# Kernel optimization log

Hardware: AMD Instinct MI355X
Metric: run time of the kernel (lower is better)

The kernel has to match this reference:

```python
import jax, jax.numpy as jnp
import numpy as np

D = 300      # d_model / entity_embed_size, hard-coded in the module
TOPK = 20    # k in torch.topk


def setup_inputs() -> dict:
    key = jax.random.key(0)
    ks = jax.random.split(key, 6)
    N, T = 2, 4096
    scale = 1.0 / np.sqrt(D).astype(np.float32)
    return {
        "querys": jax.random.normal(ks[0], (N, T, D), jnp.float32),
        "keys":   jax.random.normal(ks[1], (N, T, D), jnp.float32),
        "values": jax.random.normal(ks[2], (N, T, D), jnp.float32),
        "Wq": jax.random.normal(ks[3], (D, D), jnp.float32) * scale,
        "Wk": jax.random.normal(ks[4], (D, D), jnp.float32) * scale,
        "Wv": jax.random.normal(ks[5], (D, D), jnp.float32) * scale,
        "num_heads": 6,
    }


def reference(querys, keys, values, Wq, Wk, Wv, num_heads):
    N, Tq, d = querys.shape
    h = int(num_heads)
    dh = d // h  # head dim (must divide; 300/6 = 50)

    # nn.Linear(bias=False): y = x @ W^T
    Q = querys @ Wq.T
    K = keys @ Wk.T
    V = values @ Wv.T  # computed but unused by the 'selected' attention, kept for fidelity

    # torch.cat(torch.split(X, dh, dim=2), dim=0): head index becomes major batch dim
    def to_heads(X):
        n, t, _ = X.shape
        return X.reshape(n, t, h, dh).transpose(2, 0, 1, 3).reshape(h * n, t, dh)

    Q_, K_ = to_heads(Q), to_heads(K)

    # scaled_dot_selected_product_attention
    scores = jnp.einsum('bqd,bkd->bqk', Q_, K_) / (dh ** 0.5)  # [hN, Tq, Tk]
    max_att = scores.max(axis=1)                                # [hN, Tk] (max over queries)
    top_vals, top_ids = jax.lax.top_k(max_att, TOPK)            # [hN, 20]
    probs = jax.nn.softmax(top_vals, axis=-1)                   # [hN, 20]
    # gather from K (not V!), matching the original code
    sel = jnp.take_along_axis(K_, top_ids[:, :, None], axis=1)  # [hN, 20, dh]
    out = jnp.sum(sel * probs[:, :, None], axis=1, keepdims=True)  # [hN, 1, dh]

    # torch.cat(torch.split(outputs, N, dim=0), dim=2): merge heads back on feature dim
    out = out.reshape(h, N, 1, dh).transpose(1, 2, 0, 3).reshape(N, 1, d)
    return out
```

## Files before the change

### kernel.cpp

```cpp
#include <hip/hip_runtime.h>
#include <hip/hip_bf16.h>
#include <math.h>

#define T      4096
#define Dm     300
#define NH     6
#define DH     50
#define NB     2
#define NBATCH 12
#define KTOP   20
#define NCAND  48
#define QC     8
#define RQC    16
#define KP     320
#define JP     304
#define NBINS  4096
#define BMAX   1024

typedef short  bs8  __attribute__((ext_vector_type(8)));
typedef float  f4   __attribute__((ext_vector_type(4)));

static __device__ __forceinline__ unsigned short f2bf(float f) {
    union { float f; unsigned u; } x{f};
    unsigned r = x.u + 0x7fffu + ((x.u >> 16) & 1u);
    return (unsigned short)(r >> 16);
}
static __device__ __forceinline__ float bf2f(unsigned short h) {
    union { unsigned u; float f; } x;
    x.u = ((unsigned)h) << 16;
    return x.f;
}
static __device__ __forceinline__ unsigned fkey(float f) {
    unsigned u = __float_as_uint(f);
    return (u & 0x80000000u) ? ~u : (u | 0x80000000u);
}

__global__ __launch_bounds__(256) void splitw_kernel(
    const float* __restrict__ Wq, const float* __restrict__ Wk,
    unsigned short* __restrict__ Wh, unsigned short* __restrict__ Wl)
{
    int idx = blockIdx.x * 256 + threadIdx.x;
    if (idx >= 2 * JP * KP) return;
    int z = idx / (JP * KP), rem = idx % (JP * KP);
    int row = rem / KP, k = rem % KP;
    const float* W = z ? Wk : Wq;
    float v = (row < 300 && k < 300) ? W[row * 300 + k] : 0.f;
    unsigned short h = f2bf(v);
    float r = v - bf2f(h);
    Wh[idx] = h;
    Wl[idx] = f2bf(r);
}

__global__ __launch_bounds__(256) void proj_mfma_kernel(
    const float* __restrict__ Xq, const float* __restrict__ Xk,
    const unsigned short* __restrict__ Wh, const unsigned short* __restrict__ Wl,
    float* __restrict__ Qt, float* __restrict__ Kt)
{
    __shared__ unsigned short Bh[16][KP + 8];
    __shared__ unsigned short Bl[16][KP + 8];

    const int z = blockIdx.z;
    const float* X  = z ? Xk : Xq;
    float*       Yt = z ? Kt : Qt;
    const unsigned short* WhB = Wh + (size_t)z * JP * KP;
    const unsigned short* WlB = Wl + (size_t)z * JP * KP;

    const int m0  = blockIdx.x * 128;
    const int j0  = blockIdx.y * 16;
    const int tid = threadIdx.x;
    const int wave = tid >> 6, lane = tid & 63;
    const int m16 = lane & 15, quad = lane >> 4;

    for (int i = tid; i < 16 * 40; i += 256) {
        int row = i / 40, c = i % 40;
        *(bs8*)&Bh[row][c * 8] = *(const bs8*)(WhB + (size_t)(j0 + row) * KP + c * 8);
        *(bs8*)&Bl[row][c * 8] = *(const bs8*)(WlB + (size_t)(j0 + row) * KP + c * 8);
    }
    __syncthreads();

    f4 acc[2] = {{0.f, 0.f, 0.f, 0.f}, {0.f, 0.f, 0.f, 0.f}};
    const int rowbase = m0 + wave * 32;

    for (int ks = 0; ks < 10; ++ks) {
        bs8 Ah[2], Al[2];
#pragma unroll
        for (int mt = 0; mt < 2; ++mt) {
            const int row = rowbase + mt * 16 + m16;
            const float* src = X + (size_t)row * 300 + ks * 32 + quad * 8;
            float f[8];
            if (ks < 9) {
                float4 a = *(const float4*)src;
                float4 c = *(const float4*)(src + 4);
                f[0] = a.x; f[1] = a.y; f[2] = a.z; f[3] = a.w;
                f[4] = c.x; f[5] = c.y; f[6] = c.z; f[7] = c.w;
            } else {
                const float* rowp = X + (size_t)row * 300;
#pragma unroll
                for (int e = 0; e < 8; ++e) {
                    int k = 288 + quad * 8 + e;
                    float v = rowp[k < 300 ? k : 299];
                    f[e] = (k < 300) ? v : 0.f;
                }
            }
#pragma unroll
            for (int e = 0; e < 8; ++e) {
                unsigned short h = f2bf(f[e]);
                float r = f[e] - bf2f(h);
                Ah[mt][e] = (short)h;
                Al[mt][e] = (short)f2bf(r);
            }
        }
        bs8 Bfh = *(const bs8*)&Bh[m16][ks * 32 + quad * 8];
        bs8 Bfl = *(const bs8*)&Bl[m16][ks * 32 + quad * 8];
#pragma unroll
        for (int mt = 0; mt < 2; ++mt) {
            acc[mt] = __builtin_amdgcn_mfma_f32_16x16x32_bf16(Ah[mt], Bfh, acc[mt], 0, 0, 0);
            acc[mt] = __builtin_amdgcn_mfma_f32_16x16x32_bf16(Al[mt], Bfh, acc[mt], 0, 0, 0);
            acc[mt] = __builtin_amdgcn_mfma_f32_16x16x32_bf16(Ah[mt], Bfl, acc[mt], 0, 0, 0);
        }
    }

    const int j = j0 + m16;
    if (j < 300) {
        const int head = j / DH, jc = j % DH;
        const int n    = m0 >> 12;
        const int tloc = (m0 & (T - 1)) + wave * 32;
        float* base = Yt + ((size_t)(head * NB + n) * DH + jc) * T;
#pragma unroll
        for (int mt = 0; mt < 2; ++mt) {
            int t = tloc + mt * 16 + quad * 4;
            *(float4*)(base + t) = make_float4(acc[mt][0], acc[mt][1], acc[mt][2], acc[mt][3]);
        }
    }
}

__global__ __launch_bounds__(256) void convert_kernel(
    const float* __restrict__ Qt, const float* __restrict__ Kt,
    unsigned short* __restrict__ Qb, unsigned short* __restrict__ Kb)
{
    const float* src = blockIdx.z ? Kt : Qt;
    unsigned short* dst = blockIdx.z ? Kb : Qb;
    const int b = blockIdx.y;
    const int t = blockIdx.x * 256 + threadIdx.x;

    unsigned short h[64];
#pragma unroll
    for (int d = 0; d < DH; ++d)
        h[d] = f2bf(src[((size_t)b * DH + d) * T + t]);
#pragma unroll
    for (int d = DH; d < 64; ++d) h[d] = 0;

    unsigned short* o = dst + ((size_t)b * T + t) * 64;
#pragma unroll
    for (int i = 0; i < 8; ++i)
        *(bs8*)(o + i * 8) = *(const bs8*)(h + i * 8);
}

__global__ __launch_bounds__(256) void score_mfma_kernel(
    const unsigned short* __restrict__ Qb, const unsigned short* __restrict__ Kb,
    float* __restrict__ pamax)
{
    __shared__ unsigned short Qlds[128][72];

    const int kb   = blockIdx.x;
    const int b    = blockIdx.y;
    const int qc   = blockIdx.z;
    const int tid  = threadIdx.x;
    const int wave = tid >> 6, lane = tid & 63;
    const int m16  = lane & 15, quad = lane >> 4;

    const int k0 = kb * 256 + wave * 64;

    bs8 Bf[4][2];
#pragma unroll
    for (int kt = 0; kt < 4; ++kt)
#pragma unroll
        for (int h = 0; h < 2; ++h)
            Bf[kt][h] = *(const bs8*)(Kb + ((size_t)(b * T + k0 + kt * 16 + m16)) * 64
                                         + quad * 8 + h * 32);

    float cmax[4];
#pragma unroll
    for (int kt = 0; kt < 4; ++kt) cmax[kt] = -INFINITY;

    for (int it = 0; it < 4; ++it) {
        const int q0 = qc * 512 + it * 128;
        __syncthreads();
#pragma unroll
        for (int i = 0; i < 4; ++i) {
            int idx = i * 256 + tid;
            int r = idx >> 3, c = idx & 7;
            *(bs8*)&Qlds[r][c * 8] =
                *(const bs8*)(Qb + ((size_t)(b * T + q0 + r)) * 64 + c * 8);
        }
        __syncthreads();

#pragma unroll
        for (int mt = 0; mt < 8; ++mt) {
            bs8 A0 = *(const bs8*)&Qlds[mt * 16 + m16][quad * 8];
            bs8 A1 = *(const bs8*)&Qlds[mt * 16 + m16][quad * 8 + 32];
#pragma unroll
            for (int kt = 0; kt < 4; ++kt) {
                f4 acc = {0.f, 0.f, 0.f, 0.f};
                acc = __builtin_amdgcn_mfma_f32_16x16x32_bf16(A0, Bf[kt][0], acc, 0, 0, 0);
                acc = __builtin_amdgcn_mfma_f32_16x16x32_bf16(A1, Bf[kt][1], acc, 0, 0, 0);
                cmax[kt] = fmaxf(cmax[kt],
                                 fmaxf(fmaxf(acc[0], acc[1]), fmaxf(acc[2], acc[3])));
            }
        }
    }

#pragma unroll
    for (int kt = 0; kt < 4; ++kt) {
        float v = cmax[kt];
        v = fmaxf(v, __shfl_xor(v, 16));
        v = fmaxf(v, __shfl_xor(v, 32));
        cmax[kt] = v;
    }
    if (lane < 16) {
#pragma unroll
        for (int kt = 0; kt < 4; ++kt)
            pamax[((size_t)qc * NBATCH + b) * T + k0 + kt * 16 + lane] = cmax[kt];
    }
}

__global__ __launch_bounds__(256) void cand_kernel(
    const float* __restrict__ pamax, int* __restrict__ cand)
{
    __shared__ float vals[T];
    __shared__ int   hist[NBINS];
    __shared__ int   part[256];
    __shared__ int   bidx[BMAX];
    __shared__ float bval[BMAX];
    __shared__ int   sh_B, sh_c1, sh_nout, sh_nb;

    const int b = blockIdx.x, tid = threadIdx.x;

    for (int i = tid; i < NBINS; i += 256) hist[i] = 0;
    if (tid == 0) { sh_nout = 0; sh_nb = 0; }
    __syncthreads();

    for (int i = tid; i < T; i += 256) {
        float m = pamax[(size_t)b * T + i];
#pragma unroll
        for (int c = 1; c < QC; ++c)
            m = fmaxf(m, pamax[((size_t)c * NBATCH + b) * T + i]);
        vals[i] = m;
        atomicAdd(&hist[fkey(m) >> 20], 1);
    }
    __syncthreads();

    {
        int s = 0;
#pragma unroll
        for (int k = 0; k < 16; ++k) s += hist[tid * 16 + k];
        part[tid] = s;
        __syncthreads();
        for (int off = 1; off < 256; off <<= 1) {
            int v = (tid + off < 256) ? part[tid + off] : 0;
            __syncthreads();
            part[tid] += v;
            __syncthreads();
        }
        int run = (tid < 255) ? part[tid + 1] : 0;
        for (int k = 15; k >= 0; --k) {
            int bin = tid * 16 + k;
            int c = hist[bin];
            if (run < NCAND && run + c >= NCAND) { sh_B = bin; sh_c1 = run; }
            run += c;
        }
    }
    __syncthreads();

    const int B = sh_B;

    for (int i = tid; i < T; i += 256) {
        int kb = (int)(fkey(vals[i]) >> 20);
        if (kb > B) {
            int p = atomicAdd(&sh_nout, 1);
            cand[b * NCAND + p] = i;
        } else if (kb == B) {
            int p = atomicAdd(&sh_nb, 1);
            if (p < BMAX) { bidx[p] = i; bval[p] = vals[i]; }
        }
    }
    __syncthreads();

    const int c1   = sh_nout;
    const int need = NCAND - c1;
    const int nb   = (sh_nb < BMAX) ? sh_nb : BMAX;
    if (tid < 64) {
        for (int l = 0; l < need; ++l) {
            float mv = -INFINITY; int mp = -1, mt = 0x7fffffff;
            for (int j = tid; j < nb; j += 64) {
                float v = bval[j]; int t = bidx[j];
                if (v > mv || (v == mv && t < mt)) { mv = v; mp = j; mt = t; }
            }
#pragma unroll
            for (int off = 32; off > 0; off >>= 1) {
                float v2 = __shfl_xor(mv, off);
                int   p2 = __shfl_xor(mp, off);
                int   t2 = __shfl_xor(mt, off);
                if (v2 > mv || (v2 == mv && t2 < mt)) { mv = v2; mp = p2; mt = t2; }
            }
            if (tid == 0)
                cand[b * NCAND + c1 + l] = (mp >= 0) ? bidx[mp] : l;
            if (mp >= 0 && tid == (mp & 63)) bval[mp] = -INFINITY;
        }
    }
}

__global__ __launch_bounds__(256) void rescore_kernel(
    const float* __restrict__ Qt, const float* __restrict__ Kt,
    const int* __restrict__ cand, float* __restrict__ rmax)
{
    __shared__ float KcT[DH][NCAND];
    __shared__ float red[4][NCAND];

    const int b = blockIdx.x, qch = blockIdx.y;
    const int tid = threadIdx.x;
    const int lane = tid & 63, wv = tid >> 6;

    for (int i = tid; i < NCAND * DH; i += 256) {
        int j = i / DH, d = i - j * DH;
        KcT[d][j] = Kt[((size_t)b * DH + d) * T + cand[b * NCAND + j]];
    }
    __syncthreads();

    const int q = qch * 256 + tid;
    float qv[DH];
#pragma unroll
    for (int d = 0; d < DH; ++d)
        qv[d] = Qt[((size_t)b * DH + d) * T + q];

    for (int g = 0; g < NCAND / 8; ++g) {
        float cm[8];
#pragma unroll
        for (int j = 0; j < 8; ++j) cm[j] = 0.f;
#pragma unroll
        for (int d = 0; d < DH; ++d) {
            float4 ka = *(const float4*)&KcT[d][g * 8];
            float4 kb = *(const float4*)&KcT[d][g * 8 + 4];
            cm[0] = fmaf(qv[d], ka.x, cm[0]);
            cm[1] = fmaf(qv[d], ka.y, cm[1]);
            cm[2] = fmaf(qv[d], ka.z, cm[2]);
            cm[3] = fmaf(qv[d], ka.w, cm[3]);
            cm[4] = fmaf(qv[d], kb.x, cm[4]);
            cm[5] = fmaf(qv[d], kb.y, cm[5]);
            cm[6] = fmaf(qv[d], kb.z, cm[6]);
            cm[7] = fmaf(qv[d], kb.w, cm[7]);
        }
#pragma unroll
        for (int j = 0; j < 8; ++j) {
            float v = cm[j];
#pragma unroll
            for (int off = 32; off > 0; off >>= 1)
                v = fmaxf(v, __shfl_xor(v, off));
            if (lane == 0) red[wv][g * 8 + j] = v;
        }
    }
    __syncthreads();

    if (tid < NCAND) {
        float v = fmaxf(fmaxf(red[0][tid], red[1][tid]),
                        fmaxf(red[2][tid], red[3][tid]));
        rmax[((size_t)qch * NBATCH + b) * NCAND + tid] = v;
    }
}

__global__ __launch_bounds__(64) void final_kernel(
    const float* __restrict__ rmax, const int* __restrict__ cand,
    const float* __restrict__ Kt, float* __restrict__ out)
{
    __shared__ float selval[KTOP];
    __shared__ int   selidx[KTOP];
    __shared__ float probs[KTOP];

    const int b = blockIdx.x;
    const int lane = threadIdx.x;

    float v = -INFINITY; int idx = 0x7fffffff;
    if (lane < NCAND) {
        v = rmax[(size_t)b * NCAND + lane];
#pragma unroll
        for (int c = 1; c < RQC; ++c)
            v = fmaxf(v, rmax[((size_t)c * NBATCH + b) * NCAND + lane]);
        v *= 0.14142135623730951f;
        idx = cand[b * NCAND + lane];
    }

    for (int l = 0; l < KTOP; ++l) {
        float mv = v; int mi = idx;
#pragma unroll
        for (int off = 32; off > 0; off >>= 1) {
            float v2 = __shfl_xor(mv, off);
            int   i2 = __shfl_xor(mi, off);
            if (v2 > mv || (v2 == mv && i2 < mi)) { mv = v2; mi = i2; }
        }
        if (idx == mi) v = -INFINITY;
        if (lane == 0) { selval[l] = mv; selidx[l] = mi; }
    }
    __syncthreads();

    if (lane == 0) {
        float m = selval[0];
        float s = 0.f;
        for (int l = 0; l < KTOP; ++l) { float e = expf(selval[l] - m); probs[l] = e; s += e; }
        float inv = 1.f / s;
        for (int l = 0; l < KTOP; ++l) probs[l] *= inv;
    }
    __syncthreads();

    if (lane < DH) {
        float acc = 0.f;
#pragma unroll
        for (int l = 0; l < KTOP; ++l)
            acc += probs[l] * Kt[((size_t)b * DH + lane) * T + selidx[l]];
        int head = b / NB, n = b % NB;
        out[n * Dm + head * DH + lane] = acc;
    }
}

extern "C" void kernel_launch(void* const* d_in, const int* in_sizes, int n_in,
                              void* d_out, int out_size, void* d_ws, size_t ws_size,
                              hipStream_t stream) {
    const float* querys = (const float*)d_in[0];
    const float* keys   = (const float*)d_in[1];
    const float* Wq     = (const float*)d_in[3];
    const float* Wk     = (const float*)d_in[4];

    float* out = (float*)d_out;
    float* ws  = (float*)d_ws;

    float* Qt    = ws;
    float* Kt    = Qt + (size_t)NBATCH * DH * T;
    float* pamax = Kt + (size_t)NBATCH * DH * T;
    float* rmax  = pamax + (size_t)QC * NBATCH * T;
    unsigned short* Qb = (unsigned short*)(rmax + (size_t)RQC * NBATCH * NCAND + 8);
    Qb = (unsigned short*)(((uintptr_t)Qb + 15) & ~(uintptr_t)15);
    unsigned short* Kb  = Qb  + (size_t)NBATCH * T * 64;
    unsigned short* Whs = Kb  + (size_t)NBATCH * T * 64;
    unsigned short* Wls = Whs + (size_t)2 * JP * KP;
    int* cand = (int*)(Wls + (size_t)2 * JP * KP);

    splitw_kernel   <<<(2 * JP * KP + 255) / 256, 256, 0, stream>>>(Wq, Wk, Whs, Wls);
    proj_mfma_kernel<<<dim3(64, JP / 16, 2), 256, 0, stream>>>(querys, keys, Whs, Wls, Qt, Kt);
    convert_kernel  <<<dim3(16, NBATCH, 2), 256, 0, stream>>>(Qt, Kt, Qb, Kb);
    score_mfma_kernel<<<dim3(16, NBATCH, QC), 256, 0, stream>>>(Qb, Kb, pamax);
    cand_kernel     <<<NBATCH, 256, 0, stream>>>(pamax, cand);
    rescore_kernel  <<<dim3(NBATCH, RQC), 256, 0, stream>>>(Qt, Kt, cand, rmax);
    final_kernel    <<<NBATCH, 64, 0, stream>>>(rmax, cand, Kt, out);
}
```

Before: 242.0 us.

## Pre-split X to bf16 hi/lo, widen projection tile, swizzle LDS in convert and score

Converts querys/keys into bf16 high/low pairs once in a dedicated split kernel, so the projection kernel loads ready-made MFMA fragments instead of redoing fp32 loads and splits for every column tile. The projection kernel now covers 32 output columns per block, with JP padded to 320 and a pre-permuted LDS layout for W, which halves how often X is re-read. The convert kernel moves to a coalesced transpose through XOR-swizzled LDS with many more blocks, and the score kernel's Q tile gets an XOR swizzle to avoid bank conflicts. The cost is an extra workspace round trip for Xh/Xl, about 21 MB written and then read back.

Result: slower. 253.7 us (+4.8%).

```diff
diff --git a/kernel.cpp b/kernel.cpp
--- a/kernel.cpp
+++ b/kernel.cpp
@@ -13,9 +13,11 @@
 #define QC     8
 #define RQC    16
 #define KP     320
-#define JP     304
+#define JP     320
 #define NBINS  4096
 #define BMAX   1024
+#define XCHUNKS (16384 * 40)
+#define WCHUNKS (2 * JP * (KP / 8))
 
 typedef short  bs8  __attribute__((ext_vector_type(8)));
 typedef float  f4   __attribute__((ext_vector_type(4)));
@@ -35,101 +37,133 @@
     return (u & 0x80000000u) ? ~u : (u | 0x80000000u);
 }
 
-__global__ __launch_bounds__(256) void splitw_kernel(
+__global__ __launch_bounds__(256) void split_kernel(
+    const float* __restrict__ querys, const float* __restrict__ keys,
     const float* __restrict__ Wq, const float* __restrict__ Wk,
+    unsigned short* __restrict__ Xh, unsigned short* __restrict__ Xl,
     unsigned short* __restrict__ Wh, unsigned short* __restrict__ Wl)
 {
-    int idx = blockIdx.x * 256 + threadIdx.x;
-    if (idx >= 2 * JP * KP) return;
-    int z = idx / (JP * KP), rem = idx % (JP * KP);
-    int row = rem / KP, k = rem % KP;
-    const float* W = z ? Wk : Wq;
-    float v = (row < 300 && k < 300) ? W[row * 300 + k] : 0.f;
-    unsigned short h = f2bf(v);
-    float r = v - bf2f(h);
-    Wh[idx] = h;
-    Wl[idx] = f2bf(r);
+    const int i = blockIdx.x * 256 + threadIdx.x;
+    float f[8];
+    unsigned short *dh, *dl;
+
+    if (i < XCHUNKS) {
+        int row = i / 40, c = i - row * 40;
+        int k0 = c * 8;
+        int z = row >> 13, r = row & 8191;
+        const float* src = (z ? keys : querys) + (size_t)r * 300;
+        if (k0 + 8 <= 300) {
+            float4 a = *(const float4*)(src + k0);
+            float4 b = *(const float4*)(src + k0 + 4);
+            f[0] = a.x; f[1] = a.y; f[2] = a.z; f[3] = a.w;
+            f[4] = b.x; f[5] = b.y; f[6] = b.z; f[7] = b.w;
+        } else {
+#pragma unroll
+            for (int e = 0; e < 8; ++e) {
+                int k = k0 + e;
+                f[e] = (k < 300) ? src[k < 300 ? k : 0] : 0.f;
+            }
+        }
+        dh = Xh + (size_t)row * KP + k0;
+        dl = Xl + (size_t)row * KP + k0;
+    } else if (i < XCHUNKS + WCHUNKS) {
+        int wi = i - XCHUNKS;
+        int z = wi / (JP * (KP / 8)), rem = wi % (JP * (KP / 8));
+        int row = rem / (KP / 8), k0 = (rem % (KP / 8)) * 8;
+        const float* W = z ? Wk : Wq;
+#pragma unroll
+        for (int e = 0; e < 8; ++e) {
+            int k = k0 + e;
+            f[e] = (row < 300 && k < 300) ? W[row * 300 + (k < 300 ? k : 0)] : 0.f;
+        }
+        dh = Wh + ((size_t)z * JP + row) * KP + k0;
+        dl = Wl + ((size_t)z * JP + row) * KP + k0;
+    } else {
+        return;
+    }
+
+    bs8 vh, vl;
+#pragma unroll
+    for (int e = 0; e < 8; ++e) {
+        unsigned short h = f2bf(f[e]);
+        float r = f[e] - bf2f(h);
+        vh[e] = (short)h;
+        vl[e] = (short)f2bf(r);
+    }
+    *(bs8*)dh = vh;
+    *(bs8*)dl = vl;
 }
 
 __global__ __launch_bounds__(256) void proj_mfma_kernel(
-    const float* __restrict__ Xq, const float* __restrict__ Xk,
+    const unsigned short* __restrict__ Xh, const unsigned short* __restrict__ Xl,
     const unsigned short* __restrict__ Wh, const unsigned short* __restrict__ Wl,
     float* __restrict__ Qt, float* __restrict__ Kt)
 {
-    __shared__ unsigned short Bh[16][KP + 8];
-    __shared__ unsigned short Bl[16][KP + 8];
-
-    const int z = blockIdx.z;
-    const float* X  = z ? Xk : Xq;
-    float*       Yt = z ? Kt : Qt;
-    const unsigned short* WhB = Wh + (size_t)z * JP * KP;
-    const unsigned short* WlB = Wl + (size_t)z * JP * KP;
-
-    const int m0  = blockIdx.x * 128;
-    const int j0  = blockIdx.y * 16;
+    __shared__ unsigned short Bfh[1280 * 8];
+    __shared__ unsigned short Bfl[1280 * 8];
+
+    const int z  = blockIdx.z;
+    float* Yt = z ? Kt : Qt;
+
+    const int j0  = blockIdx.x * 32;
+    const int m0  = blockIdx.y * 128;
     const int tid = threadIdx.x;
     const int wave = tid >> 6, lane = tid & 63;
     const int m16 = lane & 15, quad = lane >> 4;
 
-    for (int i = tid; i < 16 * 40; i += 256) {
-        int row = i / 40, c = i % 40;
-        *(bs8*)&Bh[row][c * 8] = *(const bs8*)(WhB + (size_t)(j0 + row) * KP + c * 8);
-        *(bs8*)&Bl[row][c * 8] = *(const bs8*)(WlB + (size_t)(j0 + row) * KP + c * 8);
-    }
-    __syncthreads();
-
-    f4 acc[2] = {{0.f, 0.f, 0.f, 0.f}, {0.f, 0.f, 0.f, 0.f}};
-    const int rowbase = m0 + wave * 32;
+    const unsigned short* WhB = Wh + (size_t)z * JP * KP;
+    const unsigned short* WlB = Wl + (size_t)z * JP * KP;
+
+    for (int i = tid; i < 1280; i += 256) {
+        int n16 = i & 15, q = (i >> 4) & 3, ks = (i >> 6) % 10, nt = i / 640;
+        size_t src = (size_t)(j0 + nt * 16 + n16) * KP + ks * 32 + q * 8;
+        *(bs8*)&Bfh[i * 8] = *(const bs8*)(WhB + src);
+        *(bs8*)&Bfl[i * 8] = *(const bs8*)(WlB + src);
+    }
+    __syncthreads();
+
+    f4 acc[2][2] = {{{0.f,0.f,0.f,0.f},{0.f,0.f,0.f,0.f}},
+                    {{0.f,0.f,0.f,0.f},{0.f,0.f,0.f,0.f}}};
+    const int rowbase = z * 8192 + m0 + wave * 32;
+    const unsigned short* xh = Xh + (size_t)rowbase * KP;
+    const unsigned short* xl = Xl + (size_t)rowbase * KP;
 
     for (int ks = 0; ks < 10; ++ks) {
         bs8 Ah[2], Al[2];
 #pragma unroll
         for (int mt = 0; mt < 2; ++mt) {
-            const int row = rowbase + mt * 16 + m16;
-            const float* src = X + (size_t)row * 300 + ks * 32 + quad * 8;
-            float f[8];
-            if (ks < 9) {
-                float4 a = *(const float4*)src;
-                float4 c = *(const float4*)(src + 4);
-                f[0] = a.x; f[1] = a.y; f[2] = a.z; f[3] = a.w;
-                f[4] = c.x; f[5] = c.y; f[6] = c.z; f[7] = c.w;
-            } else {
-                const float* rowp = X + (size_t)row * 300;
-#pragma unroll
-                for (int e = 0; e < 8; ++e) {
-                    int k = 288 + quad * 8 + e;
-                    float v = rowp[k < 300 ? k : 299];
-                    f[e] = (k < 300) ? v : 0.f;
-                }
+            size_t off = (size_t)(mt * 16 + m16) * KP + ks * 32 + quad * 8;
+            Ah[mt] = *(const bs8*)(xh + off);
+            Al[mt] = *(const bs8*)(xl + off);
+        }
+#pragma unroll
+        for (int nt = 0; nt < 2; ++nt) {
+            int ci = (((nt * 10 + ks) * 4 + quad) * 16 + m16) * 8;
+            bs8 Bfh_ = *(const bs8*)&Bfh[ci];
+            bs8 Bfl_ = *(const bs8*)&Bfl[ci];
+#pragma unroll
+            for (int mt = 0; mt < 2; ++mt) {
+                acc[mt][nt] = __builtin_amdgcn_mfma_f32_16x16x32_bf16(Ah[mt], Bfh_, acc[mt][nt], 0, 0, 0);
+                acc[mt][nt] = __builtin_amdgcn_mfma_f32_16x16x32_bf16(Al[mt], Bfh_, acc[mt][nt], 0, 0, 0);
+                acc[mt][nt] = __builtin_amdgcn_mfma_f32_16x16x32_bf16(Ah[mt], Bfl_, acc[mt][nt], 0, 0, 0);
             }
-#pragma unroll
-            for (int e = 0; e < 8; ++e) {
-                unsigned short h = f2bf(f[e]);
-                float r = f[e] - bf2f(h);
-                Ah[mt][e] = (short)h;
-                Al[mt][e] = (short)f2bf(r);
+        }
+    }
+
+    const int n    = m0 >> 12;
+    const int tloc = (m0 & (T - 1)) + wave * 32;
+#pragma unroll
+    for (int nt = 0; nt < 2; ++nt) {
+        const int j = j0 + nt * 16 + m16;
+        if (j < 300) {
+            const int head = j / DH, jc = j % DH;
+            float* base = Yt + ((size_t)(head * NB + n) * DH + jc) * T;
+#pragma unroll
+            for (int mt = 0; mt < 2; ++mt) {
+                int t = tloc + mt * 16 + quad * 4;
+                *(float4*)(base + t) =
+                    make_float4(acc[mt][nt][0], acc[mt][nt][1], acc[mt][nt][2], acc[mt][nt][3]);
             }
-        }
-        bs8 Bfh = *(const bs8*)&Bh[m16][ks * 32 + quad * 8];
-        bs8 Bfl = *(const bs8*)&Bl[m16][ks * 32 + quad * 8];
-#pragma unroll
-        for (int mt = 0; mt < 2; ++mt) {
-            acc[mt] = __builtin_amdgcn_mfma_f32_16x16x32_bf16(Ah[mt], Bfh, acc[mt], 0, 0, 0);
-            acc[mt] = __builtin_amdgcn_mfma_f32_16x16x32_bf16(Al[mt], Bfh, acc[mt], 0, 0, 0);
-            acc[mt] = __builtin_amdgcn_mfma_f32_16x16x32_bf16(Ah[mt], Bfl, acc[mt], 0, 0, 0);
-        }
-    }
-
-    const int j = j0 + m16;
-    if (j < 300) {
-        const int head = j / DH, jc = j % DH;
-        const int n    = m0 >> 12;
-        const int tloc = (m0 & (T - 1)) + wave * 32;
-        float* base = Yt + ((size_t)(head * NB + n) * DH + jc) * T;
-#pragma unroll
-        for (int mt = 0; mt < 2; ++mt) {
-            int t = tloc + mt * 16 + quad * 4;
-            *(float4*)(base + t) = make_float4(acc[mt][0], acc[mt][1], acc[mt][2], acc[mt][3]);
         }
     }
 }
@@ -138,29 +172,38 @@
     const float* __restrict__ Qt, const float* __restrict__ Kt,
     unsigned short* __restrict__ Qb, unsigned short* __restrict__ Kb)
 {
+    __shared__ unsigned short S[32 * 8 * 8];
+
     const float* src = blockIdx.z ? Kt : Qt;
     unsigned short* dst = blockIdx.z ? Kb : Qb;
-    const int b = blockIdx.y;
-    const int t = blockIdx.x * 256 + threadIdx.x;
-
-    unsigned short h[64];
-#pragma unroll
-    for (int d = 0; d < DH; ++d)
-        h[d] = f2bf(src[((size_t)b * DH + d) * T + t]);
-#pragma unroll
-    for (int d = DH; d < 64; ++d) h[d] = 0;
-
-    unsigned short* o = dst + ((size_t)b * T + t) * 64;
-#pragma unroll
-    for (int i = 0; i < 8; ++i)
-        *(bs8*)(o + i * 8) = *(const bs8*)(h + i * 8);
+    const int b  = blockIdx.y;
+    const int t0 = blockIdx.x * 32;
+    const int tid = threadIdx.x;
+
+    {
+        const int r = tid & 31, c = tid >> 5;
+        const int ch = r * 8 + (c ^ (r & 7));
+#pragma unroll
+        for (int e = 0; e < 8; ++e) {
+            int d = c * 8 + e;
+            float v = (d < DH) ? src[((size_t)b * DH + d) * T + t0 + r] : 0.f;
+            S[ch * 8 + e] = f2bf(v);
+        }
+    }
+    __syncthreads();
+
+    {
+        const int r2 = tid >> 3, c2 = tid & 7;
+        const int ch = r2 * 8 + (c2 ^ (r2 & 7));
+        *(bs8*)(dst + ((size_t)b * T + t0 + r2) * 64 + c2 * 8) = *(const bs8*)&S[ch * 8];
+    }
 }
 
 __global__ __launch_bounds__(256) void score_mfma_kernel(
     const unsigned short* __restrict__ Qb, const unsigned short* __restrict__ Kb,
     float* __restrict__ pamax)
 {
-    __shared__ unsigned short Qlds[128][72];
+    __shared__ unsigned short Qlds[1024 * 8];
 
     const int kb   = blockIdx.x;
     const int b    = blockIdx.y;
@@ -189,16 +232,18 @@
 #pragma unroll
         for (int i = 0; i < 4; ++i) {
             int idx = i * 256 + tid;
-            int r = idx >> 3, c = idx & 7;
-            *(bs8*)&Qlds[r][c * 8] =
-                *(const bs8*)(Qb + ((size_t)(b * T + q0 + r)) * 64 + c * 8);
+            int r = idx >> 3, c2 = idx & 7;
+            int ch = r * 8 + (c2 ^ (r & 7));
+            *(bs8*)&Qlds[ch * 8] =
+                *(const bs8*)(Qb + ((size_t)(b * T + q0 + r)) * 64 + c2 * 8);
         }
         __syncthreads();
 
 #pragma unroll
         for (int mt = 0; mt < 8; ++mt) {
-            bs8 A0 = *(const bs8*)&Qlds[mt * 16 + m16][quad * 8];
-            bs8 A1 = *(const bs8*)&Qlds[mt * 16 + m16][quad * 8 + 32];
+            const int row = mt * 16 + m16;
+            bs8 A0 = *(const bs8*)&Qlds[(row * 8 + (quad ^ (row & 7))) * 8];
+            bs8 A1 = *(const bs8*)&Qlds[(row * 8 + ((quad + 4) ^ (row & 7))) * 8];
 #pragma unroll
             for (int kt = 0; kt < 4; ++kt) {
                 f4 acc = {0.f, 0.f, 0.f, 0.f};
@@ -439,13 +484,16 @@
     unsigned short* Qb = (unsigned short*)(rmax + (size_t)RQC * NBATCH * NCAND + 8);
     Qb = (unsigned short*)(((uintptr_t)Qb + 15) & ~(uintptr_t)15);
     unsigned short* Kb  = Qb  + (size_t)NBATCH * T * 64;
-    unsigned short* Whs = Kb  + (size_t)NBATCH * T * 64;
+    unsigned short* Xh  = Kb  + (size_t)NBATCH * T * 64;
+    unsigned short* Xl  = Xh  + (size_t)16384 * KP;
+    unsigned short* Whs = Xl  + (size_t)16384 * KP;
     unsigned short* Wls = Whs + (size_t)2 * JP * KP;
     int* cand = (int*)(Wls + (size_t)2 * JP * KP);
 
-    splitw_kernel   <<<(2 * JP * KP + 255) / 256, 256, 0, stream>>>(Wq, Wk, Whs, Wls);
-    proj_mfma_kernel<<<dim3(64, JP / 16, 2), 256, 0, stream>>>(querys, keys, Whs, Wls, Qt, Kt);
-    convert_kernel  <<<dim3(16, NBATCH, 2), 256, 0, stream>>>(Qt, Kt, Qb, Kb);
+    const int splitBlocks = (XCHUNKS + WCHUNKS + 255) / 256;
+    split_kernel    <<<splitBlocks, 256, 0, stream>>>(querys, keys, Wq, Wk, Xh, Xl, Whs, Wls);
+    proj_mfma_kernel<<<dim3(10, 64, 2), 256, 0, stream>>>(Xh, Xl, Whs, Wls, Qt, Kt);
+    convert_kernel  <<<dim3(128, NBATCH, 2), 256, 0, stream>>>(Qt, Kt, Qb, Kb);
     score_mfma_kernel<<<dim3(16, NBATCH, QC), 256, 0, stream>>>(Qb, Kb, pamax);
     cand_kernel     <<<NBATCH, 256, 0, stream>>>(pamax, cand);
     rescore_kernel  <<<dim3(NBATCH, RQC), 256, 0, stream>>>(Qt, Kt, cand, rmax);
```
